# Performance work log

Hardware: AMD Instinct MI355X
Metric: run time of the kernel (lower is better)

The kernel has to match this reference:

```python
import jax, jax.numpy as jnp
import numpy as np

N_USERS = 250000
N_ITEMS = 250000
D = 64          # embedding_dim
H = 64          # hidden_dim
N_EDGES = 1200000
N_NODES = N_USERS + N_ITEMS


def gcn_conv(x, W, b, src, dst, num_nodes):
    """PyG-style GCNConv: add self-loops, symmetric deg normalization, scatter-add."""
    loop = jnp.arange(num_nodes, dtype=src.dtype)
    s = jnp.concatenate([src, loop])
    d = jnp.concatenate([dst, loop])
    deg = jax.ops.segment_sum(jnp.ones(d.shape, x.dtype), d, num_segments=num_nodes)
    dinv = deg ** -0.5  # deg >= 1 thanks to self-loops
    h = x @ W  # [N, H]
    norm = dinv[s] * dinv[d]  # [E']
    msg = h[s] * norm[:, None]  # [E', H] gather
    out = jax.ops.segment_sum(msg, d, num_segments=num_nodes)  # scatter-add
    return out + b


def setup_inputs() -> dict:
    key = jax.random.key(0)
    ks = jax.random.split(key, 8)
    inp = {
        "user_table": jax.random.normal(ks[0], (N_USERS, D), jnp.float32) * 0.1,
        "item_table": jax.random.normal(ks[1], (N_ITEMS, D), jnp.float32) * 0.1,
        "W1": jax.random.normal(ks[2], (D, H), jnp.float32) * (1.0 / np.sqrt(D)),
        "b1": jnp.zeros((H,), jnp.float32),
        "W2": jax.random.normal(ks[3], (H, H), jnp.float32) * (1.0 / np.sqrt(H)),
        "b2": jnp.zeros((H,), jnp.float32),
        "Wp": jax.random.normal(ks[4], (2 * H, 1), jnp.float32) * (1.0 / np.sqrt(2 * H)),
        "bp": jnp.zeros((1,), jnp.float32),
        "edge_index": jax.random.randint(ks[5], (2, N_EDGES), 0, N_NODES, jnp.int32),
        "user_ids": jax.random.randint(ks[6], (N_USERS,), 0, N_USERS, jnp.int32),
        "item_ids": jax.random.randint(ks[7], (N_ITEMS,), 0, N_ITEMS, jnp.int32),
    }
    return inp


def reference(user_table, item_table, W1, b1, W2, b2, Wp, bp,
              edge_index, user_ids, item_ids):
    # embedding bag lookups (one id per bag -> plain gather)
    user_emb = user_table[user_ids]   # [num_users, D]
    item_emb = item_table[item_ids]   # [num_items, D]
    x = jnp.concatenate([user_emb, item_emb], axis=0)  # [N_NODES, D]

    src, dst = edge_index[0], edge_index[1]
    x = jax.nn.relu(gcn_conv(x, W1, b1, src, dst, N_NODES))
    x = jax.nn.relu(gcn_conv(x, W2, b2, src, dst, N_NODES))

    u = x[:N_USERS][user_ids]   # [B, H]
    i = x[N_USERS:][item_ids]   # [B, H]
    combined = jnp.concatenate([u, i], axis=1)  # [B, 2H]
    return combined @ Wp + bp   # [B, 1]
```

## Files before the change

kernel.cpp:

```cpp
#include <hip/hip_runtime.h>

#define NUSERS 250000
#define NITEMS 250000
#define NNODES 500000
#define NEDGES 1200000
#define NGROUPS (NNODES/16)
#define NCH8   (NNODES/8)

#define NB     245
#define BCAP   6144
#define SEGE   8192
#define NBLKA  147

typedef _Float16 half_t;
typedef _Float16 half8 __attribute__((ext_vector_type(8)));
typedef _Float16 half4 __attribute__((ext_vector_type(4)));
typedef float    f32x4 __attribute__((ext_vector_type(4)));


__global__ void k_zero_gc(int* __restrict__ gc) {
    int t = threadIdx.x;
    if (t < NB) gc[t] = 0;
}

__global__ __launch_bounds__(256) void k_bucketA(
    const int* __restrict__ src, const int* __restrict__ dst,
    int* __restrict__ gcursor, unsigned int* __restrict__ gbuf)
{
    __shared__ int ecnt[256];
    __shared__ int ebase[256];
    __shared__ int ecur[256];
    __shared__ int gres[256];
    __shared__ unsigned int stage[SEGE];
    __shared__ unsigned char stb[SEGE];

    const int t = threadIdx.x;
    const int e0 = blockIdx.x * SEGE;
    const int ecount = min(SEGE, NEDGES - e0);

    ecnt[t] = 0;
    __syncthreads();
    for (int k = t; k < ecount; k += 256)
        atomicAdd(&ecnt[dst[e0 + k] >> 11], 1);
    __syncthreads();

    const int v = ecnt[t];
    ebase[t] = v; __syncthreads();
    for (int d = 1; d < 256; d <<= 1) {
        int x = (t >= d) ? ebase[t - d] : 0;
        __syncthreads();
        ebase[t] += x;
        __syncthreads();
    }
    const int excl = ebase[t] - v;
    __syncthreads();
    ebase[t] = excl;
    ecur[t]  = excl;
    if (t < NB && v > 0) gres[t] = atomicAdd(&gcursor[t], v);
    __syncthreads();

    for (int k = t; k < ecount; k += 256) {
        const int s  = src[e0 + k];
        const int d2 = dst[e0 + k];
        const int b  = d2 >> 11;
        const int p  = atomicAdd(&ecur[b], 1);
        stage[p] = ((unsigned int)s << 11) | (unsigned int)(d2 & 2047);
        stb[p]   = (unsigned char)b;
    }
    __syncthreads();

    for (int s = t; s < ecount; s += 256) {
        const int b = stb[s];
        gbuf[(size_t)b * BCAP + gres[b] + (s - ebase[b])] = stage[s];
    }
}

__global__ __launch_bounds__(256) void k_scan_buckets(const int* __restrict__ gcursor,
                                                      int* __restrict__ bbase)
{
    __shared__ int sm[256];
    const int t = threadIdx.x;
    const int v = (t < NB) ? gcursor[t] : 0;
    sm[t] = v; __syncthreads();
    for (int d = 1; d < 256; d <<= 1) {
        int x = (t >= d) ? sm[t - d] : 0;
        __syncthreads();
        sm[t] += x;
        __syncthreads();
    }
    if (t < NB) bbase[t] = sm[t] - v;
}

__global__ __launch_bounds__(256) void k_bucketB(
    const int* __restrict__ gcursor, const int* __restrict__ bbase,
    const unsigned int* __restrict__ gbuf,
    float* __restrict__ dinv, int* __restrict__ offsets, int* __restrict__ csr)
{
    __shared__ int hist[2048];
    __shared__ int cur[2048];
    __shared__ int psum[256];
    __shared__ int lcsr[BCAP];

    const int t = threadIdx.x;
    const int b = blockIdx.x;
    const int cnt = gcursor[b];
    const int nbase = b << 11;
    const int nb = min(2048, NNODES - nbase);
    const unsigned int* gb0 = gbuf + (size_t)b * BCAP;
    const int cbase = bbase[b];

    for (int i = t; i < 2048; i += 256) hist[i] = 0;
    __syncthreads();
    for (int s = t; s < cnt; s += 256)
        atomicAdd(&hist[gb0[s] & 2047], 1);
    __syncthreads();

    for (int i = t; i < nb; i += 256)
        dinv[nbase + i] = 1.0f / sqrtf((float)(hist[i] + 1));

    int loc[8]; int ssum = 0;
#pragma unroll
    for (int k = 0; k < 8; ++k) { loc[k] = hist[t * 8 + k]; ssum += loc[k]; }
    psum[t] = ssum; __syncthreads();
    for (int d = 1; d < 256; d <<= 1) {
        int x = (t >= d) ? psum[t - d] : 0;
        __syncthreads();
        psum[t] += x;
        __syncthreads();
    }
    int run = psum[t] - ssum;
#pragma unroll
    for (int k = 0; k < 8; ++k) {
        const int i = t * 8 + k;
        if (i < nb) offsets[nbase + i] = cbase + run;
        cur[i] = run;
        run += loc[k];
    }
    __syncthreads();
    if (b == NB - 1 && t == 0) offsets[NNODES] = cbase + cnt;

    for (int s = t; s < cnt; s += 256) {
        const unsigned int pk = gb0[s];
        const int p = atomicAdd(&cur[pk & 2047], 1);
        lcsr[p] = (int)(pk >> 11);
    }
    __syncthreads();
    for (int s = t; s < cnt; s += 256)
        csr[cbase + s] = lcsr[s];
}


__device__ __forceinline__ void build_bfrags(const float* __restrict__ W,
                                             int lg, int cl, half8 bf[2][4]) {
#pragma unroll
    for (int q = 0; q < 2; ++q)
#pragma unroll
        for (int c = 0; c < 4; ++c) {
            half8 v;
#pragma unroll
            for (int j = 0; j < 8; ++j)
                v[j] = (half_t)W[(32 * q + 8 * lg + j) * 64 + 4 * cl + c];
            bf[q][c] = v;
        }
}


__global__ __launch_bounds__(256) void k_mm1(
    const float* __restrict__ user_table, const float* __restrict__ item_table,
    const int* __restrict__ uid, const int* __restrict__ iid,
    const float* __restrict__ W1, const float* __restrict__ dinv,
    half_t* __restrict__ g)
{
    const int lane = threadIdx.x & 63;
    const int lg = lane >> 4, cl = lane & 15;
    const int wid = blockIdx.x * (blockDim.x >> 6) + (threadIdx.x >> 6);
    const int nw  = gridDim.x * (blockDim.x >> 6);

    half8 bf[2][4];
    build_bfrags(W1, lg, cl, bf);
    const f32x4 zacc = {0.f, 0.f, 0.f, 0.f};

    int t = wid;
    f32x4 u0, u1, u2, u3;
    if (t < NGROUPS) {
        const int na = t * 16 + cl;
        const float* p = (na < NUSERS)
            ? user_table + (size_t)uid[na] * 64
            : item_table + (size_t)iid[na - NUSERS] * 64;
        u0 = *(const f32x4*)(p + 8 * lg);
        u1 = *(const f32x4*)(p + 8 * lg + 4);
        u2 = *(const f32x4*)(p + 8 * lg + 32);
        u3 = *(const f32x4*)(p + 8 * lg + 36);
    }
    while (t < NGROUPS) {
        const int tn = t + nw;
        const int tl = (tn < NGROUPS) ? tn : t;
        const int nb2 = tl * 16 + cl;
        const float* pn = (nb2 < NUSERS)
            ? user_table + (size_t)uid[nb2] * 64
            : item_table + (size_t)iid[nb2 - NUSERS] * 64;
        f32x4 v0 = *(const f32x4*)(pn + 8 * lg);
        f32x4 v1 = *(const f32x4*)(pn + 8 * lg + 4);
        f32x4 v2 = *(const f32x4*)(pn + 8 * lg + 32);
        f32x4 v3 = *(const f32x4*)(pn + 8 * lg + 36);

        const int n0 = t * 16;
        half8 a0, a1;
#pragma unroll
        for (int j = 0; j < 4; ++j) {
            a0[j] = (half_t)u0[j]; a0[4 + j] = (half_t)u1[j];
            a1[j] = (half_t)u2[j]; a1[4 + j] = (half_t)u3[j];
        }
        f32x4 acc[4];
#pragma unroll
        for (int c = 0; c < 4; ++c) {
            acc[c] = __builtin_amdgcn_mfma_f32_16x16x32_f16(a0, bf[0][c], zacc, 0, 0, 0);
            acc[c] = __builtin_amdgcn_mfma_f32_16x16x32_f16(a1, bf[1][c], acc[c], 0, 0, 0);
        }
#pragma unroll
        for (int r = 0; r < 4; ++r) {
            const int nd = n0 + lg * 4 + r;
            const float dn = dinv[nd];
            half4 hv;
#pragma unroll
            for (int c = 0; c < 4; ++c) hv[c] = (half_t)(acc[c][r] * dn);
            *(half4*)(g + (size_t)nd * 64 + 4 * cl) = hv;
        }
        u0 = v0; u1 = v1; u2 = v2; u3 = v3;
        t = tn;
    }
}


__global__ __launch_bounds__(256) void k_gather_mm2(
    const int* __restrict__ off, const int* __restrict__ csr,
    const float* __restrict__ W2, const float* __restrict__ b1,
    const float* __restrict__ dinv,
    const half_t* __restrict__ g1, half_t* __restrict__ g2)
{
    const int lane = threadIdx.x & 63;
    const int lg = lane >> 4, cl = lane & 15;
    const int wid = blockIdx.x * (blockDim.x >> 6) + (threadIdx.x >> 6);
    const int nw  = gridDim.x * (blockDim.x >> 6);

    half8 bf[2][4];
    build_bfrags(W2, lg, cl, bf);
    float bias0[8], bias1[8];
#pragma unroll
    for (int j = 0; j < 8; ++j) {
        bias0[j] = b1[8 * lg + j];
        bias1[j] = b1[32 + 8 * lg + j];
    }
    const f32x4 zacc = {0.f, 0.f, 0.f, 0.f};

    for (int t = wid; t < NGROUPS; t += nw) {
        const int n0 = t * 16;
        const int n  = n0 + cl;
        const int eb = off[n];
        const int deg = off[n + 1] - eb;

        float f0[8], f1[8];
        {
            half8 s0 = *(const half8*)(g1 + (size_t)n * 64 + 8 * lg);
            half8 s1 = *(const half8*)(g1 + (size_t)n * 64 + 32 + 8 * lg);
#pragma unroll
            for (int j = 0; j < 8; ++j) { f0[j] = (float)s0[j]; f1[j] = (float)s1[j]; }
        }

        int md = deg;
        md = max(md, __shfl_xor(md, 1, 64));
        md = max(md, __shfl_xor(md, 2, 64));
        md = max(md, __shfl_xor(md, 4, 64));
        md = max(md, __shfl_xor(md, 8, 64));

        for (int ss = 0; ss < md; ss += 4) {
            const bool v0 = ss < deg,     v1 = ss + 1 < deg;
            const bool v2 = ss + 2 < deg, v3 = ss + 3 < deg;
            const int p0 = csr[v0 ? eb + ss     : 0];
            const int p1 = csr[v1 ? eb + ss + 1 : 0];
            const int p2 = csr[v2 ? eb + ss + 2 : 0];
            const int p3 = csr[v3 ? eb + ss + 3 : 0];
            const half8 r00 = *(const half8*)(g1 + (size_t)p0 * 64 + 8 * lg);
            const half8 r01 = *(const half8*)(g1 + (size_t)p0 * 64 + 32 + 8 * lg);
            const half8 r10 = *(const half8*)(g1 + (size_t)p1 * 64 + 8 * lg);
            const half8 r11 = *(const half8*)(g1 + (size_t)p1 * 64 + 32 + 8 * lg);
            const half8 r20 = *(const half8*)(g1 + (size_t)p2 * 64 + 8 * lg);
            const half8 r21 = *(const half8*)(g1 + (size_t)p2 * 64 + 32 + 8 * lg);
            const half8 r30 = *(const half8*)(g1 + (size_t)p3 * 64 + 8 * lg);
            const half8 r31 = *(const half8*)(g1 + (size_t)p3 * 64 + 32 + 8 * lg);
            const float m0 = v0 ? 1.0f : 0.0f;
            const float m1 = v1 ? 1.0f : 0.0f;
            const float m2 = v2 ? 1.0f : 0.0f;
            const float m3 = v3 ? 1.0f : 0.0f;
#pragma unroll
            for (int j = 0; j < 8; ++j) {
                f0[j] = fmaf(m0, (float)r00[j], f0[j]);
                f1[j] = fmaf(m0, (float)r01[j], f1[j]);
            }
#pragma unroll
            for (int j = 0; j < 8; ++j) {
                f0[j] = fmaf(m1, (float)r10[j], f0[j]);
                f1[j] = fmaf(m1, (float)r11[j], f1[j]);
            }
#pragma unroll
            for (int j = 0; j < 8; ++j) {
                f0[j] = fmaf(m2, (float)r20[j], f0[j]);
                f1[j] = fmaf(m2, (float)r21[j], f1[j]);
            }
#pragma unroll
            for (int j = 0; j < 8; ++j) {
                f0[j] = fmaf(m3, (float)r30[j], f0[j]);
                f1[j] = fmaf(m3, (float)r31[j], f1[j]);
            }
        }

        const float dna = dinv[n];
        half8 a0, a1;
#pragma unroll
        for (int j = 0; j < 8; ++j) {
            a0[j] = (half_t)fmaxf(fmaf(dna, f0[j], bias0[j]), 0.0f);
            a1[j] = (half_t)fmaxf(fmaf(dna, f1[j], bias1[j]), 0.0f);
        }
        f32x4 acc[4];
#pragma unroll
        for (int c = 0; c < 4; ++c) {
            acc[c] = __builtin_amdgcn_mfma_f32_16x16x32_f16(a0, bf[0][c], zacc, 0, 0, 0);
            acc[c] = __builtin_amdgcn_mfma_f32_16x16x32_f16(a1, bf[1][c], acc[c], 0, 0, 0);
        }
#pragma unroll
        for (int r = 0; r < 4; ++r) {
            const int nd = n0 + lg * 4 + r;
            const float dn = dinv[nd];
            half4 hv;
#pragma unroll
            for (int c = 0; c < 4; ++c) hv[c] = (half_t)(acc[c][r] * dn);
            *(half4*)(g2 + (size_t)nd * 64 + 4 * cl) = hv;
        }
    }
}


#define G8_STEP(K)                                                            \
        const bool v##K = sstep + K < deg;                                    \
        const int p##K = csr[v##K ? eb + sstep + K : 0];

#define G8_ROW(K)                                                             \
        const half8 r##K = *(const half8*)(g_p + (size_t)p##K * 64 + sub * 8);

#define G8_ACC(K) {                                                           \
        const float m_ = v##K ? 1.0f : 0.0f;                                  \
        acc0 = fmaf(m_, (float)r##K[0], acc0); acc1 = fmaf(m_, (float)r##K[1], acc1); \
        acc2 = fmaf(m_, (float)r##K[2], acc2); acc3 = fmaf(m_, (float)r##K[3], acc3); \
        acc4 = fmaf(m_, (float)r##K[4], acc4); acc5 = fmaf(m_, (float)r##K[5], acc5); \
        acc6 = fmaf(m_, (float)r##K[6], acc6); acc7 = fmaf(m_, (float)r##K[7], acc7); }

#define GATHER_G8(ginp)                                                       \
    const half_t* __restrict__ g_p = (ginp);                                  \
    const int n  = n0 + gi;                                                   \
    const int eb = off[n];                                                    \
    const int deg = off[n + 1] - eb;                                          \
    float acc0, acc1, acc2, acc3, acc4, acc5, acc6, acc7;                     \
    {                                                                         \
        half8 sv = *(const half8*)(g_p + (size_t)n * 64 + sub * 8);           \
        acc0 = (float)sv[0]; acc1 = (float)sv[1];                             \
        acc2 = (float)sv[2]; acc3 = (float)sv[3];                             \
        acc4 = (float)sv[4]; acc5 = (float)sv[5];                             \
        acc6 = (float)sv[6]; acc7 = (float)sv[7];                             \
    }                                                                         \
    int md = deg;                                                             \
    md = max(md, __shfl_xor(md, 8, 64));                                      \
    md = max(md, __shfl_xor(md, 16, 64));                                     \
    md = max(md, __shfl_xor(md, 32, 64));                                     \
    for (int sstep = 0; sstep < md; sstep += 8) {                             \
        G8_STEP(0) G8_STEP(1) G8_STEP(2) G8_STEP(3)                           \
        G8_STEP(4) G8_STEP(5) G8_STEP(6) G8_STEP(7)                           \
        G8_ROW(0) G8_ROW(1) G8_ROW(2) G8_ROW(3)                               \
        G8_ROW(4) G8_ROW(5) G8_ROW(6) G8_ROW(7)                               \
        G8_ACC(0) G8_ACC(1) G8_ACC(2) G8_ACC(3)                               \
        G8_ACC(4) G8_ACC(5) G8_ACC(6) G8_ACC(7)                               \
    }

__global__ __launch_bounds__(256) void k_gather_ps(
    const int* __restrict__ off, const int* __restrict__ csr,
    const float* __restrict__ b2, const float* __restrict__ Wp,
    const float* __restrict__ dinv,
    const half_t* __restrict__ g2, float* __restrict__ pscore)
{
    const int lane = threadIdx.x & 63;
    const int gi = lane >> 3;
    const int sub = lane & 7;
    const int wid = blockIdx.x * (blockDim.x >> 6) + (threadIdx.x >> 6);
    const int nw  = gridDim.x * (blockDim.x >> 6);

    float bb[8], wpu[8], wpi[8];
#pragma unroll
    for (int k = 0; k < 8; ++k) {
        bb[k]  = b2[sub * 8 + k];
        wpu[k] = Wp[sub * 8 + k];
        wpi[k] = Wp[64 + sub * 8 + k];
    }

    for (int t = wid; t < NCH8; t += nw) {
        const int n0 = t * 8;
        GATHER_G8(g2)

        const bool isu = (n0 < NUSERS);
        const float dn = dinv[n];
        float v = 0.0f;
#define PS_ACC(K, A) {                                                      \
        float w_ = isu ? wpu[K] : wpi[K];                                   \
        float x_ = fmaxf(fmaf(dn, (A), bb[K]), 0.0f);                       \
        v = fmaf(x_, w_, v); }
        PS_ACC(0, acc0) PS_ACC(1, acc1) PS_ACC(2, acc2) PS_ACC(3, acc3)
        PS_ACC(4, acc4) PS_ACC(5, acc5) PS_ACC(6, acc6) PS_ACC(7, acc7)
#undef PS_ACC
        v += __shfl_xor(v, 1, 64);
        v += __shfl_xor(v, 2, 64);
        v += __shfl_xor(v, 4, 64);
        if (sub == 0) pscore[n] = v;
    }
}

__global__ void k_pairs(const int* __restrict__ user_ids, const int* __restrict__ item_ids,
                        const float* __restrict__ pscore, const float* __restrict__ bp,
                        float* __restrict__ out)
{
    int b = blockIdx.x * blockDim.x + threadIdx.x;
    if (b < NUSERS)
        out[b] = pscore[user_ids[b]] + pscore[NUSERS + item_ids[b]] + bp[0];
}


extern "C" void kernel_launch(void* const* d_in, const int* in_sizes, int n_in,
                              void* d_out, int out_size, void* d_ws, size_t ws_size,
                              hipStream_t stream)
{
    const float* user_table = (const float*)d_in[0];
    const float* item_table = (const float*)d_in[1];
    const float* W1 = (const float*)d_in[2];
    const float* b1 = (const float*)d_in[3];
    const float* W2 = (const float*)d_in[4];
    const float* b2 = (const float*)d_in[5];
    const float* Wp = (const float*)d_in[6];
    const float* bp = (const float*)d_in[7];
    const int* edge = (const int*)d_in[8];
    const int* uid  = (const int*)d_in[9];
    const int* iid  = (const int*)d_in[10];
    float* out = (float*)d_out;

    const int* src = edge;
    const int* dst = edge + NEDGES;

    char* ws = (char*)d_ws;
    float*        pscore   = (float*)       (ws + 0);
    float*        dinv     = (float*)       (ws + 2000000);
    int*          offsets  = (int*)         (ws + 4000000);
    int*          bbase    = (int*)         (ws + 6000128);
    int*          gcursor  = (int*)         (ws + 6004224);
    int*          csr      = (int*)         (ws + 6008000);
    half_t*       bufA     = (half_t*)      (ws + 10808064);
    half_t*       bufB     = (half_t*)      (ws + 74808064);
    unsigned int* gbuf     = (unsigned int*)(ws + 74808064);

    k_zero_gc     <<<1, 256, 0, stream>>>(gcursor);
    k_bucketA     <<<NBLKA, 256, 0, stream>>>(src, dst, gcursor, gbuf);
    k_scan_buckets<<<1, 256, 0, stream>>>(gcursor, bbase);
    k_bucketB     <<<NB, 256, 0, stream>>>(gcursor, bbase, gbuf, dinv, offsets, csr);

    k_mm1       <<<2048, 256, 0, stream>>>(user_table, item_table, uid, iid, W1, dinv, bufA);
    k_gather_mm2<<<2048, 256, 0, stream>>>(offsets, csr, W2, b1, dinv, bufA, bufB);
    k_gather_ps <<<2048, 256, 0, stream>>>(offsets, csr, b2, Wp, dinv, bufB, pscore);
    k_pairs     <<<(NUSERS + 255) / 256, 256, 0, stream>>>(uid, iid, pscore, bp, out);
}
```

Before: 195.9 us.

## Sort nodes by degree within buckets to balance gather work per wavefront

The bucket kernel now counting-sorts each 2048-node bucket by in-degree (capped at 31) and writes a node permutation. Both gather kernels process nodes in that permuted order, so lanes in one wavefront have similar degrees and spend fewer loop iterations on masked-out edges. Output rows are written through the permuted node ids, which makes the stores scattered rather than contiguous, and each group now needs an extra indirection load. Grid sizes for the three main kernels are also doubled.

```diff
diff --git a/kernel.cpp b/kernel.cpp
--- a/kernel.cpp
+++ b/kernel.cpp
@@ -94,11 +94,13 @@
 __global__ __launch_bounds__(256) void k_bucketB(
     const int* __restrict__ gcursor, const int* __restrict__ bbase,
     const unsigned int* __restrict__ gbuf,
-    float* __restrict__ dinv, int* __restrict__ offsets, int* __restrict__ csr)
+    float* __restrict__ dinv, int* __restrict__ offsets, int* __restrict__ csr,
+    int* __restrict__ perm)
 {
     __shared__ int hist[2048];
     __shared__ int cur[2048];
     __shared__ int psum[256];
+    __shared__ int dcnt[32];
     __shared__ int lcsr[BCAP];
 
     const int t = threadIdx.x;
@@ -110,6 +112,7 @@
     const int cbase = bbase[b];
 
     for (int i = t; i < 2048; i += 256) hist[i] = 0;
+    if (t < 32) dcnt[t] = 0;
     __syncthreads();
     for (int s = t; s < cnt; s += 256)
         atomicAdd(&hist[gb0[s] & 2047], 1);
@@ -147,6 +150,19 @@
     __syncthreads();
     for (int s = t; s < cnt; s += 256)
         csr[cbase + s] = lcsr[s];
+
+    for (int i = t; i < nb; i += 256)
+        atomicAdd(&dcnt[min(hist[i], 31)], 1);
+    __syncthreads();
+    if (t == 0) {
+        int r2 = 0;
+        for (int k = 0; k < 32; ++k) { int c = dcnt[k]; dcnt[k] = r2; r2 += c; }
+    }
+    __syncthreads();
+    for (int i = t; i < nb; i += 256) {
+        int pos = atomicAdd(&dcnt[min(hist[i], 31)], 1);
+        perm[nbase + pos] = nbase + i;
+    }
 }
 
 
@@ -234,6 +250,7 @@
 
 __global__ __launch_bounds__(256) void k_gather_mm2(
     const int* __restrict__ off, const int* __restrict__ csr,
+    const int* __restrict__ perm,
     const float* __restrict__ W2, const float* __restrict__ b1,
     const float* __restrict__ dinv,
     const half_t* __restrict__ g1, half_t* __restrict__ g2)
@@ -255,7 +272,7 @@
 
     for (int t = wid; t < NGROUPS; t += nw) {
         const int n0 = t * 16;
-        const int n  = n0 + cl;
+        const int n  = perm[n0 + cl];
         const int eb = off[n];
         const int deg = off[n + 1] - eb;
 
@@ -329,7 +346,7 @@
         }
 #pragma unroll
         for (int r = 0; r < 4; ++r) {
-            const int nd = n0 + lg * 4 + r;
+            const int nd = __shfl(n, lg * 4 + r, 64);
             const float dn = dinv[nd];
             half4 hv;
 #pragma unroll
@@ -354,9 +371,9 @@
         acc4 = fmaf(m_, (float)r##K[4], acc4); acc5 = fmaf(m_, (float)r##K[5], acc5); \
         acc6 = fmaf(m_, (float)r##K[6], acc6); acc7 = fmaf(m_, (float)r##K[7], acc7); }
 
-#define GATHER_G8(ginp)                                                       \
+#define GATHER_G8(ginp, NODE)                                                 \
     const half_t* __restrict__ g_p = (ginp);                                  \
-    const int n  = n0 + gi;                                                   \
+    const int n  = (NODE);                                                    \
     const int eb = off[n];                                                    \
     const int deg = off[n + 1] - eb;                                          \
     float acc0, acc1, acc2, acc3, acc4, acc5, acc6, acc7;                     \
@@ -382,6 +399,7 @@
 
 __global__ __launch_bounds__(256) void k_gather_ps(
     const int* __restrict__ off, const int* __restrict__ csr,
+    const int* __restrict__ perm,
     const float* __restrict__ b2, const float* __restrict__ Wp,
     const float* __restrict__ dinv,
     const half_t* __restrict__ g2, float* __restrict__ pscore)
@@ -402,9 +420,9 @@
 
     for (int t = wid; t < NCH8; t += nw) {
         const int n0 = t * 8;
-        GATHER_G8(g2)
-
-        const bool isu = (n0 < NUSERS);
+        GATHER_G8(g2, perm[n0 + gi])
+
+        const bool isu = (n < NUSERS);
         const float dn = dinv[n];
         float v = 0.0f;
 #define PS_ACC(K, A) {                                                      \
@@ -460,15 +478,16 @@
     int*          csr      = (int*)         (ws + 6008000);
     half_t*       bufA     = (half_t*)      (ws + 10808064);
     half_t*       bufB     = (half_t*)      (ws + 74808064);
+    int*          perm     = (int*)         (ws + 138808064);
     unsigned int* gbuf     = (unsigned int*)(ws + 74808064);
 
     k_zero_gc     <<<1, 256, 0, stream>>>(gcursor);
     k_bucketA     <<<NBLKA, 256, 0, stream>>>(src, dst, gcursor, gbuf);
     k_scan_buckets<<<1, 256, 0, stream>>>(gcursor, bbase);
-    k_bucketB     <<<NB, 256, 0, stream>>>(gcursor, bbase, gbuf, dinv, offsets, csr);
-
-    k_mm1       <<<2048, 256, 0, stream>>>(user_table, item_table, uid, iid, W1, dinv, bufA);
-    k_gather_mm2<<<2048, 256, 0, stream>>>(offsets, csr, W2, b1, dinv, bufA, bufB);
-    k_gather_ps <<<2048, 256, 0, stream>>>(offsets, csr, b2, Wp, dinv, bufB, pscore);
+    k_bucketB     <<<NB, 256, 0, stream>>>(gcursor, bbase, gbuf, dinv, offsets, csr, perm);
+
+    k_mm1       <<<4096, 256, 0, stream>>>(user_table, item_table, uid, iid, W1, dinv, bufA);
+    k_gather_mm2<<<4096, 256, 0, stream>>>(offsets, csr, perm, W2, b1, dinv, bufA, bufB);
+    k_gather_ps <<<4096, 256, 0, stream>>>(offsets, csr, perm, b2, Wp, dinv, bufB, pscore);
     k_pairs     <<<(NUSERS + 255) / 256, 256, 0, stream>>>(uid, iid, pscore, bp, out);
 }
```

Measured after the change: 241.7 us. +23.4%, slower.
